# Optimization experiments

Hardware: AMD Instinct MI355X
Metric: run time of the kernel (lower is better)

The kernel has to match this reference:

```python
import jax, jax.numpy as jnp
import numpy as np

N, E, D, A, M, H, NRES = 65536, 16384, 1024, 512, 2048, 3, 3


def setup_inputs() -> dict:
    key = jax.random.key(0)
    ks = jax.random.split(key, 24)
    s = 0.02
    inp = {
        'h': jax.random.normal(ks[0], (N, D), dtype=jnp.float32),
        'rep': jax.random.normal(ks[1], (N, D), dtype=jnp.float32),
        'src': jax.random.randint(ks[2], (E,), 0, N, dtype=jnp.int32),
        'dst': jax.random.randint(ks[3], (E,), 0, N, dtype=jnp.int32),
        # per-head attention projections (stacked over H heads)
        'Wq': s * jax.random.normal(ks[4], (H, D, A), dtype=jnp.float32),
        'bq': s * jax.random.normal(ks[5], (H, A), dtype=jnp.float32),
        'Wk': s * jax.random.normal(ks[6], (H, D, A), dtype=jnp.float32),
        'bk': s * jax.random.normal(ks[7], (H, A), dtype=jnp.float32),
        'Wv': s * jax.random.normal(ks[8], (H, D, A), dtype=jnp.float32),
        'bv': s * jax.random.normal(ks[9], (H, A), dtype=jnp.float32),
        # MultiMLPLayer: first Linear(A->M), then NRES ResNet blocks of width M
        'W0': s * jax.random.normal(ks[10], (H, A, M), dtype=jnp.float32),
        'b0': s * jax.random.normal(ks[11], (H, M), dtype=jnp.float32),
        'Wr': s * jax.random.normal(ks[12], (H, NRES, M, M), dtype=jnp.float32),
        'br': s * jax.random.normal(ks[13], (H, NRES, M), dtype=jnp.float32),
        'g_ln': jnp.ones((H, NRES, M), dtype=jnp.float32),
        'b_ln': jnp.zeros((H, NRES, M), dtype=jnp.float32),
        # mlp_scale: Linear(M->A) per head
        'Wms': s * jax.random.normal(ks[14], (H, M, A), dtype=jnp.float32),
        'bms': s * jax.random.normal(ks[15], (H, A), dtype=jnp.float32),
        # update_attn_scale: Linear(H*A -> D, bias=False)
        'Wuas': s * jax.random.normal(ks[16], (H * A, D), dtype=jnp.float32),
    }
    return inp


def _layernorm(x, g, b, eps=1e-5):
    mu = jnp.mean(x, axis=-1, keepdims=True)
    var = jnp.mean((x - mu) ** 2, axis=-1, keepdims=True)
    return (x - mu) / jnp.sqrt(var + eps) * g + b


def reference(h, rep, src, dst, Wq, bq, Wk, bk, Wv, bv, W0, b0, Wr, br,
              g_ln, b_ln, Wms, bms, Wuas):
    # model normalizes all node embeddings first (F.normalize)
    hn = h / jnp.maximum(jnp.linalg.norm(h, axis=-1, keepdims=True), 1e-12)
    Q = hn[src]            # [E, D] mailbox messages (copy_u of 'h')
    K = rep[dst]           # [E, D] destination node reps (K == V)

    # per-head projections: [H, E, A]
    Qp = jnp.einsum('ed,hda->hea', Q, Wq) + bq[:, None, :]
    Kp = jnp.einsum('ed,hda->hea', K, Wk) + bk[:, None, :]
    Vp = jnp.einsum('ed,hda->hea', K, Wv) + bv[:, None, :]

    attn_dim = Wq.shape[-1]
    scores = (Qp * Kp) / (attn_dim ** 0.5)       # 2D path: elementwise QK, scaled by sqrt(attn_size)
    attn = jax.nn.softmax(scores, axis=-1)       # softmax over feature dim
    attn_out = attn * Vp                         # [H, E, A] (dropout p=0.0 in TreeHopNode)

    # MultiMLPLayer: Linear(A->M) then NRES ResNet blocks
    m = jnp.einsum('hea,ham->hem', attn_out, W0) + b0[:, None, :]
    for j in range(Wr.shape[1]):
        xn = _layernorm(m, g_ln[:, j][:, None, :], b_ln[:, j][:, None, :])
        m = m + jax.nn.relu(jnp.einsum('hem,hmn->hen', xn, Wr[:, j]) + br[:, j][:, None, :])

    head_out = jnp.einsum('hem,hma->hea', m, Wms) + bms[:, None, :] + attn_out  # [H, E, A]
    cat = jnp.transpose(head_out, (1, 0, 2)).reshape(Q.shape[0], -1)            # [E, H*A]

    # reduce_func: h = Q - K + update_attn_scale(multi_head_out)
    return Q - K + cat @ Wuas                                                   # [E, D]
```

## Files before the change

kernel.cpp:

```cpp
#include <hip/hip_runtime.h>
#include <hip/hip_bf16.h>
#include <cstdint>
#include <cstddef>

typedef __bf16 bf16;
typedef __bf16 bf16x2 __attribute__((ext_vector_type(2)));
typedef __bf16 bf16x4 __attribute__((ext_vector_type(4)));
typedef __bf16 bf16x8 __attribute__((ext_vector_type(8)));
typedef float f32x4 __attribute__((ext_vector_type(4)));

static_assert(sizeof(bf16x8) == 16, "bf16x8 must be 16B");

#define NE 16384
#define ND 1024
#define NA 512
#define NM 2048
#define NH 3
#define NRES 3

__device__ __forceinline__ void async_ld16(const bf16* g, bf16* l) {
  __builtin_amdgcn_global_load_lds(
      (__attribute__((address_space(1))) void*)(void*)g,
      (__attribute__((address_space(3))) void*)(void*)l, 16, 0, 0);
}

template <int N>
__device__ __forceinline__ void vm_wait() {
  asm volatile("s_waitcnt vmcnt(%0)" ::"n"(N) : "memory");
}
__device__ __forceinline__ void bar() {
  asm volatile("s_barrier" ::: "memory");
}


#define LDA_Q(BUF, MQ)                                                        \
  {                                                                           \
    const int ab_ = ((BUF)*2 + (MQ)) * 8192 + aOff;                           \
    _Pragma("unroll") for (int ks = 0; ks < 2; ++ks) {                        \
      const int co_ = (c0 ^ (ks << 2)) * 8;                                   \
      _Pragma("unroll") for (int i = 0; i < 4; ++i)                           \
          fa[ks][i] = *(const bf16x8*)&lA[ab_ + i * 1024 + co_];              \
    }                                                                         \
  }

#define LDB_Q(DST, BUF, NQ)                                                   \
  {                                                                           \
    const int bb_ = ((BUF)*2 + (NQ)) * 8192 + bOff;                           \
    _Pragma("unroll") for (int ks = 0; ks < 2; ++ks) {                        \
      const int co_ = (c0 ^ (ks << 2)) * 8;                                   \
      _Pragma("unroll") for (int j = 0; j < 2; ++j)                           \
          DST[ks][j] = *(const bf16x8*)&lB[bb_ + j * 1024 + co_];             \
    }                                                                         \
  }

#define MFMA_Q(MQ, NQ, FB)                                                    \
  __builtin_amdgcn_s_setprio(1);                                              \
  _Pragma("unroll") for (int ks = 0; ks < 2; ++ks)                            \
  _Pragma("unroll") for (int i = 0; i < 4; ++i)                               \
  _Pragma("unroll") for (int j = 0; j < 2; ++j)                               \
      acc[(MQ)*4 + i][(NQ)*2 + j] = __builtin_amdgcn_mfma_f32_16x16x32_bf16(  \
          fa[ks][i], FB[ks][j], acc[(MQ)*4 + i][(NQ)*2 + j], 0, 0, 0);        \
  __builtin_amdgcn_s_setprio(0);

template <int MODE>
__global__ __launch_bounds__(512, 2) void gemm_kernel(
    const bf16* __restrict__ A, const bf16* __restrict__ B,
    const float* __restrict__ bias, void* __restrict__ Cv,
    const bf16* __restrict__ addb, int K, int ldc, int coloff, int addld,
    int nby) {
  __shared__ bf16 lA[32768];
  __shared__ bf16 lB[32768];

  const int nwg = gridDim.x;
  int bid = blockIdx.x;
  if ((nwg & 7) == 0) bid = (bid & 7) * (nwg >> 3) + (bid >> 3);
  const int m0 = (bid % nby) * 256;
  const int n0 = (bid / nby) * 256;

  const int tid = threadIdx.x;
  const int wv = tid >> 6, ln = tid & 63;
  const int wm = wv >> 2, wn = wv & 3;

  const int rowq = wv * 8 + (ln >> 3);
  const int colo = ((ln & 7) ^ (ln >> 3)) * 8;
  const bf16* gA = A + (size_t)(m0 + rowq) * K + colo;
  const bf16* gB = B + (size_t)(n0 + rowq) * K + colo;

  auto stageA = [&](int bf, int u, int t) {
#pragma unroll
    for (int r = 0; r < 2; ++r)
      async_ld16(gA + (size_t)(r * 128 + u * 64) * K + t * 64,
                 &lA[((bf * 2 + u) * 128 + r * 64 + wv * 8) * 64]);
  };
  auto stageB = [&](int bf, int u, int t) {
#pragma unroll
    for (int r = 0; r < 2; ++r)
      async_ld16(gB + (size_t)(r * 128 + u * 64) * K + t * 64,
                 &lB[((bf * 2 + u) * 128 + r * 64 + wv * 8) * 64]);
  };

  const int l15 = ln & 15;
  const int aOff = (wm * 64 + l15) * 64;
  const int bOff = (wn * 32 + l15) * 64;
  const int c0 = (ln >> 4) ^ (ln & 7);

  f32x4 acc[8][4] = {};
  bf16x8 fa[2][4], fb0[2][2], fb1[2][2];

  const int nt = K >> 6;

  stageA(0, 0, 0); stageB(0, 0, 0); stageA(0, 1, 0); stageB(0, 1, 0);
  stageA(1, 0, 1); stageB(1, 0, 1); stageA(1, 1, 1); stageB(1, 1, 1);
  vm_wait<8>();
  bar();
  LDB_Q(fb0, 0, 0);

  for (int t = 0; t < nt; ++t) {
    const int buf = t & 1, nb = buf ^ 1;
    const bool s1 = t + 1 < nt, s2 = t + 2 < nt;
    LDA_Q(buf, 0);
    if (s2) stageB(buf, 0, t + 2);
    bar();
    MFMA_Q(0, 0, fb0);
    bar();
    LDB_Q(fb1, buf, 1);
    if (s2) stageA(buf, 0, t + 2);
    bar();
    MFMA_Q(0, 1, fb1);
    bar();
    LDA_Q(buf, 1);
    if (s2) stageB(buf, 1, t + 2);
    bar();
    MFMA_Q(1, 1, fb1);
    bar();
    if (s2) { stageA(buf, 1, t + 2); vm_wait<8>(); }
    else if (s1) { vm_wait<0>(); }
    bar();
    MFMA_Q(1, 0, fb0);
    if (s1) LDB_Q(fb0, nb, 0);
    bar();
  }

  const int r4 = (ln >> 4) * 4;
  const int nbase = n0 + (wn >> 1) * 128 + (wn & 1) * 32 + l15;
#pragma unroll
  for (int mi = 0; mi < 8; ++mi) {
#pragma unroll
    for (int ni = 0; ni < 4; ++ni) {
#pragma unroll
      for (int r = 0; r < 4; ++r) {
        const int m = m0 + wm * 128 + mi * 16 + r4 + r;
        const int n = nbase + (ni >> 1) * 64 + (ni & 1) * 16;
        float v = acc[mi][ni][r];
        if constexpr (MODE != 3) v += bias[n];
        if constexpr (MODE == 0) {
          ((bf16*)Cv)[(size_t)m * ldc + n] = (bf16)v;
        } else if constexpr (MODE == 1) {
          float prev = (float)addb[(size_t)m * addld + n];
          ((bf16*)Cv)[(size_t)m * ldc + n] = (bf16)(prev + fmaxf(v, 0.f));
        } else if constexpr (MODE == 2) {
          v += (float)addb[(size_t)m * addld + n];
          ((bf16*)Cv)[(size_t)m * ldc + coloff + n] = (bf16)v;
        } else {
          float* C = (float*)Cv;
          const size_t idx = (size_t)m * ldc + n;
          C[idx] = C[idx] + v;
        }
      }
    }
  }
}

template <int MODE>
static void launch_gemm(hipStream_t s, const bf16* A, const bf16* B,
                        const float* bias, void* C, const bf16* addb, int M,
                        int N, int K, int ldc, int coloff, int addld) {
  const int nby = M / 256;
  gemm_kernel<MODE><<<dim3((N / 256) * nby), 512, 0, s>>>(
      A, B, bias, C, addb, K, ldc, coloff, addld, nby);
}

__global__ void transpose_cvt(const float* __restrict__ src,
                              bf16* __restrict__ dst, int K, int N) {
  __shared__ float t[32][33];
  const size_t zo = (size_t)blockIdx.z * K * N;
  src += zo;
  dst += zo;
  const int n = blockIdx.x * 32 + threadIdx.x;
  const int kb = blockIdx.y * 32;
#pragma unroll
  for (int i = 0; i < 4; ++i) {
    const int k = kb + threadIdx.y + i * 8;
    t[threadIdx.y + i * 8][threadIdx.x] = src[(size_t)k * N + n];
  }
  __syncthreads();
#pragma unroll
  for (int i = 0; i < 4; ++i) {
    const int nn = blockIdx.x * 32 + threadIdx.y + i * 8;
    dst[(size_t)nn * K + kb + threadIdx.x] =
        (bf16)t[threadIdx.x][threadIdx.y + i * 8];
  }
}

__global__ __launch_bounds__(256) void gather_kernel(
    const float* __restrict__ h, const float* __restrict__ rep,
    const int* __restrict__ src, const int* __restrict__ dst,
    bf16* __restrict__ Qb, bf16* __restrict__ Kb, float* __restrict__ qk) {
  __shared__ float sm[4];
  const int e = blockIdx.x, tid = threadIdx.x;
  const int sr = src[e], dr = dst[e];
  const float4 hv = ((const float4*)(h + (size_t)sr * ND))[tid];
  float ss = hv.x * hv.x + hv.y * hv.y + hv.z * hv.z + hv.w * hv.w;
#pragma unroll
  for (int o = 32; o > 0; o >>= 1) ss += __shfl_down(ss, o, 64);
  if ((tid & 63) == 0) sm[tid >> 6] = ss;
  __syncthreads();
  const float tot = sm[0] + sm[1] + sm[2] + sm[3];
  const float inv = 1.f / fmaxf(sqrtf(tot), 1e-12f);
  const float4 rv = ((const float4*)(rep + (size_t)dr * ND))[tid];
  const float q0 = hv.x * inv, q1 = hv.y * inv, q2 = hv.z * inv,
              q3 = hv.w * inv;
  const size_t base = (size_t)e * ND + tid * 4;
  bf16x4 qv;
  qv[0] = (bf16)q0; qv[1] = (bf16)q1; qv[2] = (bf16)q2; qv[3] = (bf16)q3;
  *(bf16x4*)(Qb + base) = qv;
  bf16x4 kv;
  kv[0] = (bf16)rv.x; kv[1] = (bf16)rv.y; kv[2] = (bf16)rv.z;
  kv[3] = (bf16)rv.w;
  *(bf16x4*)(Kb + base) = kv;
  *(float4*)(qk + base) =
      make_float4(q0 - rv.x, q1 - rv.y, q2 - rv.z, q3 - rv.w);
}

__global__ __launch_bounds__(256) void softmax_kernel(
    const bf16* __restrict__ Qp, const bf16* __restrict__ Kp,
    const bf16* __restrict__ Vp, bf16* __restrict__ attn) {
  __shared__ float sm[4];
  const int tid = threadIdx.x;
  const int e = blockIdx.x, hh = blockIdx.y;
  const size_t base = (size_t)e * (NH * NA) + (size_t)hh * NA + 2 * tid;
  const bf16x2 q = *(const bf16x2*)(Qp + base);
  const bf16x2 k = *(const bf16x2*)(Kp + base);
  const bf16x2 v = *(const bf16x2*)(Vp + base);
  const float sc = 0.044194173824159216f;
  const float s0 = (float)q[0] * (float)k[0] * sc;
  const float s1 = (float)q[1] * (float)k[1] * sc;
  float mx = fmaxf(s0, s1);
#pragma unroll
  for (int o = 32; o > 0; o >>= 1) mx = fmaxf(mx, __shfl_down(mx, o, 64));
  if ((tid & 63) == 0) sm[tid >> 6] = mx;
  __syncthreads();
  mx = fmaxf(fmaxf(sm[0], sm[1]), fmaxf(sm[2], sm[3]));
  __syncthreads();
  const float p0 = expf(s0 - mx), p1 = expf(s1 - mx);
  float ssum = p0 + p1;
#pragma unroll
  for (int o = 32; o > 0; o >>= 1) ssum += __shfl_down(ssum, o, 64);
  if ((tid & 63) == 0) sm[tid >> 6] = ssum;
  __syncthreads();
  const float inv = 1.f / (sm[0] + sm[1] + sm[2] + sm[3]);
  bf16x2 r;
  r[0] = (bf16)(p0 * inv * (float)v[0]);
  r[1] = (bf16)(p1 * inv * (float)v[1]);
  const size_t obase = (size_t)hh * NE * NA + (size_t)e * NA + 2 * tid;
  *(bf16x2*)(attn + obase) = r;
}

__global__ __launch_bounds__(256) void ln_kernel(const bf16* __restrict__ x,
                                                 bf16* __restrict__ y,
                                                 const float* __restrict__ g,
                                                 const float* __restrict__ b) {
  __shared__ float sm[8];
  const int tid = threadIdx.x;
  const size_t base = (size_t)blockIdx.x * NM + tid * 8;
  const bf16x8 xv = *(const bf16x8*)(x + base);
  float xf[8], s = 0.f, ss = 0.f;
#pragma unroll
  for (int i = 0; i < 8; ++i) {
    xf[i] = (float)xv[i];
    s += xf[i];
    ss += xf[i] * xf[i];
  }
#pragma unroll
  for (int o = 32; o > 0; o >>= 1) {
    s += __shfl_down(s, o, 64);
    ss += __shfl_down(ss, o, 64);
  }
  if ((tid & 63) == 0) {
    sm[tid >> 6] = s;
    sm[4 + (tid >> 6)] = ss;
  }
  __syncthreads();
  s = sm[0] + sm[1] + sm[2] + sm[3];
  ss = sm[4] + sm[5] + sm[6] + sm[7];
  const float mu = s * (1.f / NM);
  const float var = ss * (1.f / NM) - mu * mu;
  const float rstd = rsqrtf(fmaxf(var, 0.f) + 1e-5f);
  const int c0 = tid * 8;
  bf16x8 yv;
#pragma unroll
  for (int i = 0; i < 8; ++i)
    yv[i] = (bf16)((xf[i] - mu) * rstd * g[c0 + i] + b[c0 + i]);
  *(bf16x8*)(y + base) = yv;
}

extern "C" void kernel_launch(void* const* d_in, const int* in_sizes, int n_in,
                              void* d_out, int out_size, void* d_ws,
                              size_t ws_size, hipStream_t stream) {
  const float* h    = (const float*)d_in[0];
  const float* rep  = (const float*)d_in[1];
  const int* src    = (const int*)d_in[2];
  const int* dst    = (const int*)d_in[3];
  const float* Wq   = (const float*)d_in[4];
  const float* bq   = (const float*)d_in[5];
  const float* Wk   = (const float*)d_in[6];
  const float* bk   = (const float*)d_in[7];
  const float* Wv   = (const float*)d_in[8];
  const float* bv   = (const float*)d_in[9];
  const float* W0   = (const float*)d_in[10];
  const float* b0   = (const float*)d_in[11];
  const float* Wr   = (const float*)d_in[12];
  const float* br   = (const float*)d_in[13];
  const float* g_ln = (const float*)d_in[14];
  const float* b_ln = (const float*)d_in[15];
  const float* Wms  = (const float*)d_in[16];
  const float* bms  = (const float*)d_in[17];
  const float* Wuas = (const float*)d_in[18];
  float* out = (float*)d_out;

  bf16* ws = (bf16*)d_ws;
  size_t off = 0;
  auto alloc = [&](size_t n) {
    bf16* p = ws + off;
    off += n;
    return p;
  };
  bf16* WqT   = alloc((size_t)NH * NA * ND);
  bf16* WkT   = alloc((size_t)NH * NA * ND);
  bf16* WvT   = alloc((size_t)NH * NA * ND);
  bf16* W0T   = alloc((size_t)NH * NM * NA);
  bf16* WrT   = alloc((size_t)NH * NRES * NM * NM);
  bf16* WmsT  = alloc((size_t)NH * NA * NM);
  bf16* WuasT = alloc((size_t)ND * NH * NA);
  bf16* Qb    = alloc((size_t)NE * ND);
  bf16* Kb    = alloc((size_t)NE * ND);
  bf16* Qp    = alloc((size_t)NE * NH * NA);
  bf16* Kp    = alloc((size_t)NE * NH * NA);
  bf16* Vp    = alloc((size_t)NE * NH * NA);
  bf16* attn  = alloc((size_t)NH * NE * NA);
  bf16* mbuf  = alloc((size_t)NE * NM);
  bf16* xnb   = alloc((size_t)NE * NM);
  bf16* cat   = Qp;
  if (ws_size < off * sizeof(bf16)) return;

  const dim3 tb(32, 8);
  transpose_cvt<<<dim3(NA / 32, ND / 32, NH), tb, 0, stream>>>(Wq, WqT, ND, NA);
  transpose_cvt<<<dim3(NA / 32, ND / 32, NH), tb, 0, stream>>>(Wk, WkT, ND, NA);
  transpose_cvt<<<dim3(NA / 32, ND / 32, NH), tb, 0, stream>>>(Wv, WvT, ND, NA);
  transpose_cvt<<<dim3(NM / 32, NA / 32, NH), tb, 0, stream>>>(W0, W0T, NA, NM);
  transpose_cvt<<<dim3(NM / 32, NM / 32, NH * NRES), tb, 0, stream>>>(Wr, WrT,
                                                                      NM, NM);
  transpose_cvt<<<dim3(NA / 32, NM / 32, NH), tb, 0, stream>>>(Wms, WmsT, NM,
                                                               NA);
  transpose_cvt<<<dim3(ND / 32, (NH * NA) / 32, 1), tb, 0, stream>>>(
      Wuas, WuasT, NH * NA, ND);

  gather_kernel<<<NE, 256, 0, stream>>>(h, rep, src, dst, Qb, Kb, out);

  launch_gemm<0>(stream, Qb, WqT, bq, Qp, nullptr, NE, NH * NA, ND, NH * NA,
                 0, 0);
  launch_gemm<0>(stream, Kb, WkT, bk, Kp, nullptr, NE, NH * NA, ND, NH * NA,
                 0, 0);
  launch_gemm<0>(stream, Kb, WvT, bv, Vp, nullptr, NE, NH * NA, ND, NH * NA,
                 0, 0);
  softmax_kernel<<<dim3(NE, NH), 256, 0, stream>>>(Qp, Kp, Vp, attn);

  for (int hh = 0; hh < NH; ++hh) {
    const bf16* attn_h = attn + (size_t)hh * NE * NA;
    launch_gemm<0>(stream, attn_h, W0T + (size_t)hh * NM * NA, b0 + hh * NM,
                   mbuf, nullptr, NE, NM, NA, NM, 0, 0);
    for (int j = 0; j < NRES; ++j) {
      const int hj = hh * NRES + j;
      ln_kernel<<<NE, 256, 0, stream>>>(mbuf, xnb, g_ln + (size_t)hj * NM,
                                        b_ln + (size_t)hj * NM);
      launch_gemm<1>(stream, xnb, WrT + (size_t)hj * NM * NM, br + hj * NM,
                     mbuf, mbuf, NE, NM, NM, NM, 0, NM);
    }
    launch_gemm<2>(stream, mbuf, WmsT + (size_t)hh * NA * NM, bms + hh * NA,
                   cat, attn_h, NE, NA, NM, NH * NA, hh * NA, NA);
  }
  launch_gemm<3>(stream, cat, WuasT, nullptr, out, nullptr, NE, ND, NH * NA,
                 ND, 0, 0);
}
```

Before: 2.936 ms.

## Split LDS fragment loads by k-half to interleave with MFMA groups

Splits each quarter's LDS fragment loads and MFMA blocks into two k-halves. Loads for the next half or quadrant are issued between the MFMA halves, so LDS reads overlap matrix math instead of waiting behind barriers. This also moves the global-to-LDS staging points and merges two stage calls into one barrier region. It relies on the existing buffer and barrier ordering staying race-free, and it keeps more fragment registers live at once.

```diff
diff --git a/kernel.cpp b/kernel.cpp
--- a/kernel.cpp
+++ b/kernel.cpp
@@ -33,33 +33,28 @@
 }
 
 
-#define LDA_Q(BUF, MQ)                                                        \
+#define LDA_H(KS, BUF, MQ)                                                    \
   {                                                                           \
     const int ab_ = ((BUF)*2 + (MQ)) * 8192 + aOff;                           \
-    _Pragma("unroll") for (int ks = 0; ks < 2; ++ks) {                        \
-      const int co_ = (c0 ^ (ks << 2)) * 8;                                   \
-      _Pragma("unroll") for (int i = 0; i < 4; ++i)                           \
-          fa[ks][i] = *(const bf16x8*)&lA[ab_ + i * 1024 + co_];              \
-    }                                                                         \
-  }
-
-#define LDB_Q(DST, BUF, NQ)                                                   \
+    const int co_ = (c0 ^ ((KS) << 2)) * 8;                                   \
+    _Pragma("unroll") for (int i = 0; i < 4; ++i)                             \
+        fa[KS][i] = *(const bf16x8*)&lA[ab_ + i * 1024 + co_];                \
+  }
+
+#define LDB_H(DST, KS, BUF, NQ)                                               \
   {                                                                           \
     const int bb_ = ((BUF)*2 + (NQ)) * 8192 + bOff;                           \
-    _Pragma("unroll") for (int ks = 0; ks < 2; ++ks) {                        \
-      const int co_ = (c0 ^ (ks << 2)) * 8;                                   \
-      _Pragma("unroll") for (int j = 0; j < 2; ++j)                           \
-          DST[ks][j] = *(const bf16x8*)&lB[bb_ + j * 1024 + co_];             \
-    }                                                                         \
-  }
-
-#define MFMA_Q(MQ, NQ, FB)                                                    \
+    const int co_ = (c0 ^ ((KS) << 2)) * 8;                                   \
+    _Pragma("unroll") for (int j = 0; j < 2; ++j)                             \
+        DST[KS][j] = *(const bf16x8*)&lB[bb_ + j * 1024 + co_];               \
+  }
+
+#define MFMA_H(KS, MQ, NQ, FB)                                                \
   __builtin_amdgcn_s_setprio(1);                                              \
-  _Pragma("unroll") for (int ks = 0; ks < 2; ++ks)                            \
   _Pragma("unroll") for (int i = 0; i < 4; ++i)                               \
   _Pragma("unroll") for (int j = 0; j < 2; ++j)                               \
       acc[(MQ)*4 + i][(NQ)*2 + j] = __builtin_amdgcn_mfma_f32_16x16x32_bf16(  \
-          fa[ks][i], FB[ks][j], acc[(MQ)*4 + i][(NQ)*2 + j], 0, 0, 0);        \
+          fa[KS][i], FB[KS][j], acc[(MQ)*4 + i][(NQ)*2 + j], 0, 0, 0);        \
   __builtin_amdgcn_s_setprio(0);
 
 template <int MODE>
@@ -113,31 +108,37 @@
   stageA(1, 0, 1); stageB(1, 0, 1); stageA(1, 1, 1); stageB(1, 1, 1);
   vm_wait<8>();
   bar();
-  LDB_Q(fb0, 0, 0);
+  LDB_H(fb0, 0, 0, 0); LDB_H(fb0, 1, 0, 0); LDA_H(0, 0, 0);
 
   for (int t = 0; t < nt; ++t) {
     const int buf = t & 1, nb = buf ^ 1;
     const bool s1 = t + 1 < nt, s2 = t + 2 < nt;
-    LDA_Q(buf, 0);
-    if (s2) stageB(buf, 0, t + 2);
-    bar();
-    MFMA_Q(0, 0, fb0);
-    bar();
-    LDB_Q(fb1, buf, 1);
-    if (s2) stageA(buf, 0, t + 2);
-    bar();
-    MFMA_Q(0, 1, fb1);
-    bar();
-    LDA_Q(buf, 1);
+    LDA_H(1, buf, 0);
+    bar();
+    MFMA_H(0, 0, 0, fb0);
+    LDB_H(fb1, 0, buf, 1);
+    LDB_H(fb1, 1, buf, 1);
+    MFMA_H(1, 0, 0, fb0);
+    bar();
+    if (s2) { stageB(buf, 0, t + 2); stageA(buf, 0, t + 2); }
+    bar();
+    MFMA_H(0, 0, 1, fb1);
+    LDA_H(0, buf, 1);
+    MFMA_H(1, 0, 1, fb1);
+    bar();
     if (s2) stageB(buf, 1, t + 2);
     bar();
-    MFMA_Q(1, 1, fb1);
+    MFMA_H(0, 1, 1, fb1);
+    LDA_H(1, buf, 1);
+    MFMA_H(1, 1, 1, fb1);
     bar();
     if (s2) { stageA(buf, 1, t + 2); vm_wait<8>(); }
     else if (s1) { vm_wait<0>(); }
     bar();
-    MFMA_Q(1, 0, fb0);
-    if (s1) LDB_Q(fb0, nb, 0);
+    MFMA_H(0, 1, 0, fb0);
+    if (s1) { LDB_H(fb0, 0, nb, 0); LDA_H(0, nb, 0); }
+    MFMA_H(1, 1, 0, fb0);
+    if (s1) LDB_H(fb0, 1, nb, 0);
     bar();
   }
 
```

After: 3.027 ms. 1.03x slower.
